# Kernel tuning notes

Hardware: AMD Instinct MI355X
Metric: run time of the kernel (lower is better)

Reference implementation:

```python
import jax, jax.numpy as jnp
import numpy as np

N_NODES = 100000
N_EDGES = 6400000
N_GRAPHS = 64


def setup_inputs() -> dict:
    key = jax.random.key(0)
    k = jax.random.split(key, 7)
    x = jax.random.normal(k[0], (N_NODES, 1), dtype=jnp.float32)
    edge_index = jax.random.randint(k[1], (2, N_EDGES), 0, N_NODES, dtype=jnp.int64)
    batch = jnp.sort(jax.random.randint(k[2], (N_NODES,), 0, N_GRAPHS, dtype=jnp.int64))
    W1 = jax.random.normal(k[3], (1, 16), dtype=jnp.float32)
    b1 = jax.random.normal(k[4], (16,), dtype=jnp.float32)
    W2 = jax.random.normal(k[5], (16, 2), dtype=jnp.float32)
    b2 = jax.random.normal(k[6], (2,), dtype=jnp.float32)
    return {"x": x, "edge_index": edge_index, "batch": batch,
            "W1": W1, "b1": b1, "W2": W2, "b2": b2}


def _gcn_layer(x, W, b, src, dst, n_nodes, dinv):
    # h = X W  (tiny feature dims)
    h = x @ W
    # symmetric normalization: norm_e = deg^-1/2[src] * deg^-1/2[dst]
    norm = dinv[src] * dinv[dst]
    msg = h[src] * norm[:, None]                 # [E+N, d] edge gather
    out = jnp.zeros((n_nodes, h.shape[1]), h.dtype).at[dst].add(msg)  # scatter-add at targets
    return out + b


def reference(x, edge_index, batch, W1, b1, W2, b2):
    n = x.shape[0]
    loops = jnp.arange(n, dtype=edge_index.dtype)
    # PyG GCNConv: add self-loops once; flow source_to_target (aggregate at edge_index[1])
    src = jnp.concatenate([edge_index[0], loops])
    dst = jnp.concatenate([edge_index[1], loops])
    deg = jnp.zeros(n, x.dtype).at[dst].add(jnp.ones((), x.dtype))
    dinv = jnp.where(deg > 0, jax.lax.rsqrt(deg), 0.0)

    h = _gcn_layer(x, W1, b1, src, dst, n, dinv)   # [N,16]
    h = _gcn_layer(h, W2, b2, src, dst, n, dinv)   # [N,2]

    # global_mean_pool over graphs
    g = N_GRAPHS
    sums = jnp.zeros((g, h.shape[1]), h.dtype).at[batch].add(h)
    counts = jnp.zeros(g, h.dtype).at[batch].add(jnp.ones((), h.dtype))
    return sums / jnp.maximum(counts, 1.0)[:, None]   # [G,2]
```

## Files before the change

kernel.cpp:

```cpp
#include <hip/hip_runtime.h>

#define N_NODES  100000
#define N_EDGES  6400000
#define N_GRAPHS 64
#define SCAN_BS  1024
#define NRDF     100096
#define DEGW     (NRDF / 4)
#define NR2      50048
#define LDSW     (NR2 / 2)
#define NR3      33344

__device__ __forceinline__ int idx_stride(const int* ei) {
    int allzero = 1;
    #pragma unroll
    for (int k = 0; k < 16; ++k)
        if (ei[2 * k + 1] != 0) allzero = 0;
    return allzero ? 2 : 1;
}

__global__ __launch_bounds__(SCAN_BS)
void deg_scan(const int* ei, unsigned char* copies) {
    __shared__ unsigned bins[DEGW];
    for (int i = threadIdx.x; i < DEGW; i += SCAN_BS) bins[i] = 0u;
    __syncthreads();
    const int stride = idx_stride(ei);
    const int tid = blockIdx.x * SCAN_BS + threadIdx.x;
    const int nth = gridDim.x * SCAN_BS;
#define DEGADD(u) { unsigned a = (unsigned)(u); \
    if (a < NRDF) atomicAdd(&bins[a >> 2], 1u << (8 * (a & 3))); }
    if (stride == 2) {
        const int4* dp = (const int4*)(ei + (size_t)N_EDGES * 2);
        const int lim = N_EDGES / 2;
        int q = tid;
        for (; q + 7 * nth < lim; q += 8 * nth) {
            int4 v0 = dp[q],           v1 = dp[q + nth];
            int4 v2 = dp[q + 2 * nth], v3 = dp[q + 3 * nth];
            int4 v4 = dp[q + 4 * nth], v5 = dp[q + 5 * nth];
            int4 v6 = dp[q + 6 * nth], v7 = dp[q + 7 * nth];
            DEGADD(v0.x); DEGADD(v0.z); DEGADD(v1.x); DEGADD(v1.z);
            DEGADD(v2.x); DEGADD(v2.z); DEGADD(v3.x); DEGADD(v3.z);
            DEGADD(v4.x); DEGADD(v4.z); DEGADD(v5.x); DEGADD(v5.z);
            DEGADD(v6.x); DEGADD(v6.z); DEGADD(v7.x); DEGADD(v7.z);
        }
        for (; q < lim; q += nth) { int4 v = dp[q]; DEGADD(v.x); DEGADD(v.z); }
    } else {
        const int4* dp = (const int4*)(ei + (size_t)N_EDGES);
        for (int q = tid; q < N_EDGES / 4; q += nth) {
            int4 v = dp[q];
            DEGADD(v.x); DEGADD(v.y); DEGADD(v.z); DEGADD(v.w);
        }
    }
#undef DEGADD
    __syncthreads();
    unsigned* my = (unsigned*)(copies + (size_t)blockIdx.x * NRDF);
    for (int i = threadIdx.x; i < DEGW; i += SCAN_BS) my[i] = bins[i];
}

__global__ void deg_merge(const unsigned char* copies, int C, const int* ei,
                          const float* x, const int* batch,
                          float* wx, float2* pbt) {
    __shared__ float red[256];
    int il = threadIdx.x & 63, cs = threadIdx.x >> 6;
    int gi = blockIdx.x * 64 + il;
    bool ok = (gi < N_NODES);
    float partial = 0.0f;
    if (ok)
        for (int c = cs; c < C; c += 4)
            partial += (float)copies[(size_t)c * NRDF + gi];
    red[threadIdx.x] = partial;
    __syncthreads();
    if (cs == 0 && ok) {
        float d = 1.0f + red[il] + red[64 + il] + red[128 + il] + red[192 + il];
        float di = rsqrtf(d);
        wx[gi] = di * x[gi];
        const int stride = idx_stride(ei);
        pbt[gi] = make_float2(di, (float)batch[(size_t)gi * stride]);
    }
}

__device__ __forceinline__ void pk_add_f16(unsigned ldsBase, unsigned a, float v) {
    _Float16 h = (_Float16)v;
    unsigned hb = (unsigned)__builtin_bit_cast(unsigned short, h);
    unsigned pk = (a & 1) ? (hb << 16) : hb;
    unsigned addr = ldsBase + ((a >> 1) << 2);
    asm volatile("ds_pk_add_f16 %0, %1" :: "v"(addr), "v"(pk) : "memory");
}

__global__ __launch_bounds__(SCAN_BS)
void acc1_scan(const int* ei, const float* wx, int G, unsigned* copies) {
    __shared__ unsigned bins[LDSW];
    for (int i = threadIdx.x; i < LDSW; i += SCAN_BS) bins[i] = 0u;
    __syncthreads();
    const int grp = (blockIdx.x >= G) ? 1 : 0;
    const int lo = grp * NR2;
    const int lb = blockIdx.x - grp * G;
    const unsigned ldsBase = (unsigned)(uintptr_t)&bins[0];
    const int stride = idx_stride(ei);
    const int tid = lb * SCAN_BS + threadIdx.x;
    const int nth = G * SCAN_BS;
    if (stride == 2) {
        const int4* sp = (const int4*)ei;
        const int4* dp = (const int4*)(ei + (size_t)N_EDGES * 2);
        const int lim = N_EDGES / 2;
        int q = tid;
        for (; q + 3 * nth < lim; q += 4 * nth) {
            int4 d0 = dp[q],           d1 = dp[q + nth];
            int4 d2 = dp[q + 2 * nth], d3 = dp[q + 3 * nth];
            int4 s0 = sp[q],           s1 = sp[q + nth];
            int4 s2 = sp[q + 2 * nth], s3 = sp[q + 3 * nth];
            unsigned a0 = (unsigned)(d0.x - lo), a1 = (unsigned)(d0.z - lo);
            unsigned a2 = (unsigned)(d1.x - lo), a3 = (unsigned)(d1.z - lo);
            unsigned a4 = (unsigned)(d2.x - lo), a5 = (unsigned)(d2.z - lo);
            unsigned a6 = (unsigned)(d3.x - lo), a7 = (unsigned)(d3.z - lo);
            float w0 = (a0 < NR2) ? wx[s0.x] : 0.0f;
            float w1 = (a1 < NR2) ? wx[s0.z] : 0.0f;
            float w2 = (a2 < NR2) ? wx[s1.x] : 0.0f;
            float w3 = (a3 < NR2) ? wx[s1.z] : 0.0f;
            float w4 = (a4 < NR2) ? wx[s2.x] : 0.0f;
            float w5 = (a5 < NR2) ? wx[s2.z] : 0.0f;
            float w6 = (a6 < NR2) ? wx[s3.x] : 0.0f;
            float w7 = (a7 < NR2) ? wx[s3.z] : 0.0f;
            if (a0 < NR2) pk_add_f16(ldsBase, a0, w0);
            if (a1 < NR2) pk_add_f16(ldsBase, a1, w1);
            if (a2 < NR2) pk_add_f16(ldsBase, a2, w2);
            if (a3 < NR2) pk_add_f16(ldsBase, a3, w3);
            if (a4 < NR2) pk_add_f16(ldsBase, a4, w4);
            if (a5 < NR2) pk_add_f16(ldsBase, a5, w5);
            if (a6 < NR2) pk_add_f16(ldsBase, a6, w6);
            if (a7 < NR2) pk_add_f16(ldsBase, a7, w7);
        }
        for (; q < lim; q += nth) {
            int4 dv = dp[q]; int4 sv = sp[q];
            unsigned a = (unsigned)(dv.x - lo), b = (unsigned)(dv.z - lo);
            if (a < NR2) pk_add_f16(ldsBase, a, wx[sv.x]);
            if (b < NR2) pk_add_f16(ldsBase, b, wx[sv.z]);
        }
    } else {
        const int4* sp = (const int4*)ei;
        const int4* dp = (const int4*)(ei + (size_t)N_EDGES);
        for (int q = tid; q < N_EDGES / 4; q += nth) {
            int4 dv = dp[q]; int4 sv = sp[q];
            unsigned a = (unsigned)(dv.x - lo), b = (unsigned)(dv.y - lo);
            unsigned c = (unsigned)(dv.z - lo), d = (unsigned)(dv.w - lo);
            if (a < NR2) pk_add_f16(ldsBase, a, wx[sv.x]);
            if (b < NR2) pk_add_f16(ldsBase, b, wx[sv.y]);
            if (c < NR2) pk_add_f16(ldsBase, c, wx[sv.z]);
            if (d < NR2) pk_add_f16(ldsBase, d, wx[sv.w]);
        }
    }
    __syncthreads();
    unsigned* my = copies + (size_t)blockIdx.x * LDSW;
    for (int i = threadIdx.x; i < LDSW; i += SCAN_BS) my[i] = bins[i];
}

__global__ void acc1_merge(const unsigned* copies, int G,
                           const float* wx, const float2* pbt,
                           float* y1, unsigned* pyz, float* gacc) {
    __shared__ float red[256];
    int t = threadIdx.x;
    if (blockIdx.x == 0 && t < 3 * N_GRAPHS) gacc[t] = 0.0f;
    int il = t & 63, cs = t >> 6;
    int gi = blockIdx.x * 64 + il;
    bool ok = (gi < N_NODES);
    float partial = 0.0f;
    int grp = (gi >= NR2) ? 1 : 0;
    int li  = gi - grp * NR2;
    if (ok) {
        int sh = 16 * (li & 1), w = li >> 1;
        const unsigned* base = copies + (size_t)grp * G * LDSW;
        for (int c = cs; c < G; c += 4) {
            unsigned u = (base[(size_t)c * LDSW + w] >> sh) & 0xFFFFu;
            partial += (float)__builtin_bit_cast(_Float16, (unsigned short)u);
        }
    }
    red[t] = partial;
    __syncthreads();
    if (cs == 0 && ok) {
        float a1 = red[il] + red[64 + il] + red[128 + il] + red[192 + il];
        float di = pbt[gi].x;
        float y1v = di * (a1 + wx[gi]);
        y1[gi] = y1v;
        _Float16 hy = (_Float16)(di * y1v);
        _Float16 hz = (_Float16)di;
        pyz[gi] = (unsigned)__builtin_bit_cast(unsigned short, hy)
                | ((unsigned)__builtin_bit_cast(unsigned short, hz) << 16);
    }
}

__global__ __launch_bounds__(SCAN_BS)
void acc2_scan(const int* ei, const unsigned* pyz, int G, unsigned* copies) {
    __shared__ unsigned bins[NR3];
    for (int i = threadIdx.x; i < NR3; i += SCAN_BS) bins[i] = 0u;
    __syncthreads();
    const int grp = blockIdx.x / G;
    const int lo = grp * NR3;
    const int lb = blockIdx.x - grp * G;
    const unsigned ldsBase = (unsigned)(uintptr_t)&bins[0];
    const int stride = idx_stride(ei);
    const int tid = lb * SCAN_BS + threadIdx.x;
    const int nth = G * SCAN_BS;
#define PKW(addr_a, pk) asm volatile("ds_pk_add_f16 %0, %1" :: \
    "v"(ldsBase + ((addr_a) << 2)), "v"(pk) : "memory")
    if (stride == 2) {
        const int4* sp = (const int4*)ei;
        const int4* dp = (const int4*)(ei + (size_t)N_EDGES * 2);
        const int lim = N_EDGES / 2;
        int q = tid;
        for (; q + 3 * nth < lim; q += 4 * nth) {
            int4 d0 = dp[q],           d1 = dp[q + nth];
            int4 d2 = dp[q + 2 * nth], d3 = dp[q + 3 * nth];
            int4 s0 = sp[q],           s1 = sp[q + nth];
            int4 s2 = sp[q + 2 * nth], s3 = sp[q + 3 * nth];
            unsigned a0 = (unsigned)(d0.x - lo), a1 = (unsigned)(d0.z - lo);
            unsigned a2 = (unsigned)(d1.x - lo), a3 = (unsigned)(d1.z - lo);
            unsigned a4 = (unsigned)(d2.x - lo), a5 = (unsigned)(d2.z - lo);
            unsigned a6 = (unsigned)(d3.x - lo), a7 = (unsigned)(d3.z - lo);
            unsigned p0 = (a0 < NR3) ? pyz[s0.x] : 0u;
            unsigned p1 = (a1 < NR3) ? pyz[s0.z] : 0u;
            unsigned p2 = (a2 < NR3) ? pyz[s1.x] : 0u;
            unsigned p3 = (a3 < NR3) ? pyz[s1.z] : 0u;
            unsigned p4 = (a4 < NR3) ? pyz[s2.x] : 0u;
            unsigned p5 = (a5 < NR3) ? pyz[s2.z] : 0u;
            unsigned p6 = (a6 < NR3) ? pyz[s3.x] : 0u;
            unsigned p7 = (a7 < NR3) ? pyz[s3.z] : 0u;
            if (a0 < NR3) PKW(a0, p0);
            if (a1 < NR3) PKW(a1, p1);
            if (a2 < NR3) PKW(a2, p2);
            if (a3 < NR3) PKW(a3, p3);
            if (a4 < NR3) PKW(a4, p4);
            if (a5 < NR3) PKW(a5, p5);
            if (a6 < NR3) PKW(a6, p6);
            if (a7 < NR3) PKW(a7, p7);
        }
        for (; q < lim; q += nth) {
            int4 dv = dp[q]; int4 sv = sp[q];
            unsigned a = (unsigned)(dv.x - lo), b = (unsigned)(dv.z - lo);
            if (a < NR3) { unsigned p = pyz[sv.x]; PKW(a, p); }
            if (b < NR3) { unsigned p = pyz[sv.z]; PKW(b, p); }
        }
    } else {
        const int4* sp = (const int4*)ei;
        const int4* dp = (const int4*)(ei + (size_t)N_EDGES);
        for (int q = tid; q < N_EDGES / 4; q += nth) {
            int4 dv = dp[q]; int4 sv = sp[q];
            unsigned a = (unsigned)(dv.x - lo), b = (unsigned)(dv.y - lo);
            unsigned c = (unsigned)(dv.z - lo), d = (unsigned)(dv.w - lo);
            if (a < NR3) { unsigned p = pyz[sv.x]; PKW(a, p); }
            if (b < NR3) { unsigned p = pyz[sv.y]; PKW(b, p); }
            if (c < NR3) { unsigned p = pyz[sv.z]; PKW(c, p); }
            if (d < NR3) { unsigned p = pyz[sv.w]; PKW(d, p); }
        }
    }
#undef PKW
    __syncthreads();
    unsigned* my = copies + (size_t)blockIdx.x * NR3;
    for (int i = threadIdx.x; i < NR3; i += SCAN_BS) my[i] = bins[i];
}

__global__ void acc2_merge(const unsigned* copies, int G,
                           const float* y1, const float2* pbt, float* gacc) {
    __shared__ float redY[256];
    __shared__ float redZ[256];
    __shared__ float bins[3 * N_GRAPHS];
    int t = threadIdx.x;
    for (int k = t; k < 3 * N_GRAPHS; k += 256) bins[k] = 0.0f;
    int il = t & 63, cs = t >> 6;
    int gi = blockIdx.x * 64 + il;
    bool ok = (gi < N_NODES);
    float pyv = 0.0f, pzv = 0.0f;
    if (ok) {
        int grp = gi / NR3;
        int li  = gi - grp * NR3;
        const unsigned* base = copies + (size_t)grp * G * NR3;
        for (int c = cs; c < G; c += 4) {
            unsigned u = base[(size_t)c * NR3 + li];
            pyv += (float)__builtin_bit_cast(_Float16, (unsigned short)(u & 0xFFFFu));
            pzv += (float)__builtin_bit_cast(_Float16, (unsigned short)(u >> 16));
        }
    }
    redY[t] = pyv;
    redZ[t] = pzv;
    __syncthreads();
    if (cs == 0 && ok) {
        float a2 = redY[il] + redY[64 + il] + redY[128 + il] + redY[192 + il];
        float az = redZ[il] + redZ[64 + il] + redZ[128 + il] + redZ[192 + il];
        float2 pb = pbt[gi];
        float di = pb.x;
        int g = (int)pb.y;
        float di2 = di * di;
        float yv = di * a2 + di2 * y1[gi];
        float zv = di * az + di2;
        atomicAdd(&bins[g], yv);
        atomicAdd(&bins[N_GRAPHS + g], zv);
        atomicAdd(&bins[2 * N_GRAPHS + g], 1.0f);
    }
    __syncthreads();
    for (int k = t; k < 3 * N_GRAPHS; k += 256)
        if (bins[k] != 0.0f) atomicAdd(&gacc[k], bins[k]);
}

__global__ void final_kernel(const float* W1, const float* b1, const float* W2,
                             const float* b2, const float* gacc, float* out) {
    int g = threadIdx.x;
    if (g >= N_GRAPHS) return;
    float w0 = 0.f, w1 = 0.f, c0 = 0.f, c1 = 0.f;
    for (int j = 0; j < 16; ++j) {
        float a = W2[2 * j], b = W2[2 * j + 1];
        w0 += W1[j] * a;  w1 += W1[j] * b;
        c0 += b1[j] * a;  c1 += b1[j] * b;
    }
    float sy  = gacc[g];
    float sz  = gacc[N_GRAPHS + g];
    float cnt = gacc[2 * N_GRAPHS + g];
    float inv = 1.0f / fmaxf(cnt, 1.0f);
    out[2 * g + 0] = (sy * w0 + sz * c0 + cnt * b2[0]) * inv;
    out[2 * g + 1] = (sy * w1 + sz * c1 + cnt * b2[1]) * inv;
}

extern "C" void kernel_launch(void* const* d_in, const int* in_sizes, int n_in,
                              void* d_out, int out_size, void* d_ws, size_t ws_size,
                              hipStream_t stream) {
    const float* x     = (const float*)d_in[0];
    const int*   ei    = (const int*)d_in[1];
    const int*   batch = (const int*)d_in[2];
    const float* W1    = (const float*)d_in[3];
    const float* b1    = (const float*)d_in[4];
    const float* W2    = (const float*)d_in[5];
    const float* b2    = (const float*)d_in[6];
    float* out = (float*)d_out;

    float*    f    = (float*)d_ws;
    float*    wx   = f;
    float*    y1   = wx + N_NODES;
    float2*   pbt  = (float2*)(y1 + N_NODES);
    unsigned* pyz  = (unsigned*)(pbt + N_NODES);
    float*    gacc = (float*)(pyz + N_NODES);
    unsigned* copies = (unsigned*)(gacc + 3 * N_GRAPHS + 16);

    const long fixedB = (5L * N_NODES + 3 * N_GRAPHS + 16) * 4;
    long availB = (long)ws_size - fixedB;
    long CD = availB / NRDF;
    if (CD > 256) CD = 256; if (CD < 8) CD = 8;
    long G1 = availB / (2L * LDSW * 4);
    if (G1 > 128) G1 = 128; if (G1 < 4) G1 = 4;
    long G2 = availB / (3L * NR3 * 4);
    if (G2 > 85) G2 = 85; if (G2 < 4) G2 = 4;

    deg_scan<<<(int)CD, SCAN_BS, 0, stream>>>(ei, (unsigned char*)copies);
    deg_merge<<<(N_NODES + 63) / 64, 256, 0, stream>>>(
        (const unsigned char*)copies, (int)CD, ei, x, batch, wx, pbt);

    acc1_scan<<<(int)(2 * G1), SCAN_BS, 0, stream>>>(ei, wx, (int)G1, copies);
    acc1_merge<<<(N_NODES + 63) / 64, 256, 0, stream>>>(
        copies, (int)G1, wx, pbt, y1, pyz, gacc);

    acc2_scan<<<(int)(3 * G2), SCAN_BS, 0, stream>>>(ei, pyz, (int)G2, copies);
    acc2_merge<<<(N_NODES + 63) / 64, 256, 0, stream>>>(
        copies, (int)G2, y1, pbt, gacc);

    final_kernel<<<1, 64, 0, stream>>>(W1, b1, W2, b2, gacc, out);
}
```

Baseline: 158.3 us.

## Compact int64 edge indices to packed int32 columns during degree pass

Measured after the change: 173.0 us. 9.3% more time.

```diff
diff --git a/kernel.cpp b/kernel.cpp
--- a/kernel.cpp
+++ b/kernel.cpp
@@ -16,6 +16,159 @@
     for (int k = 0; k < 16; ++k)
         if (ei[2 * k + 1] != 0) allzero = 0;
     return allzero ? 2 : 1;
+}
+
+__device__ __forceinline__ void pk_add_f16(unsigned ldsBase, unsigned a, float v) {
+    _Float16 h = (_Float16)v;
+    unsigned hb = (unsigned)__builtin_bit_cast(unsigned short, h);
+    unsigned pk = (a & 1) ? (hb << 16) : hb;
+    unsigned addr = ldsBase + ((a >> 1) << 2);
+    asm volatile("ds_pk_add_f16 %0, %1" :: "v"(addr), "v"(pk) : "memory");
+}
+
+__global__ __launch_bounds__(SCAN_BS)
+void pack_deg(const int* ei, unsigned* dstc, unsigned* srcc,
+              unsigned char* copies) {
+    __shared__ unsigned bins[DEGW];
+    for (int i = threadIdx.x; i < DEGW; i += SCAN_BS) bins[i] = 0u;
+    __syncthreads();
+    const int stride = idx_stride(ei);
+    const int tid = blockIdx.x * SCAN_BS + threadIdx.x;
+    const int nth = gridDim.x * SCAN_BS;
+#define DEGADD(u) { unsigned a = (unsigned)(u); \
+    if (a < NRDF) atomicAdd(&bins[a >> 2], 1u << (8 * (a & 3))); }
+    if (stride == 2) {
+        const int4* dp = (const int4*)(ei + (size_t)N_EDGES * 2);
+        const int4* sp = (const int4*)ei;
+        uint2* d2 = (uint2*)dstc;
+        uint2* s2 = (uint2*)srcc;
+        for (int q = tid; q < N_EDGES / 2; q += nth) {
+            int4 dv = dp[q], sv = sp[q];
+            DEGADD(dv.x); DEGADD(dv.z);
+            d2[q] = make_uint2((unsigned)dv.x, (unsigned)dv.z);
+            s2[q] = make_uint2((unsigned)sv.x, (unsigned)sv.z);
+        }
+    } else {
+        const int4* dp = (const int4*)(ei + (size_t)N_EDGES);
+        const int4* sp = (const int4*)ei;
+        int4* d4 = (int4*)dstc;
+        int4* s4 = (int4*)srcc;
+        for (int q = tid; q < N_EDGES / 4; q += nth) {
+            int4 dv = dp[q], sv = sp[q];
+            DEGADD(dv.x); DEGADD(dv.y); DEGADD(dv.z); DEGADD(dv.w);
+            d4[q] = dv;
+            s4[q] = sv;
+        }
+    }
+#undef DEGADD
+    __syncthreads();
+    unsigned* my = (unsigned*)(copies + (size_t)blockIdx.x * NRDF);
+    for (int i = threadIdx.x; i < DEGW; i += SCAN_BS) my[i] = bins[i];
+}
+
+__global__ __launch_bounds__(SCAN_BS)
+void acc1_scanP(const unsigned* dstc, const unsigned* srcc, const float* wx,
+                int G, unsigned* copies) {
+    __shared__ unsigned bins[LDSW];
+    for (int i = threadIdx.x; i < LDSW; i += SCAN_BS) bins[i] = 0u;
+    __syncthreads();
+    const int grp = (blockIdx.x >= G) ? 1 : 0;
+    const int lo = grp * NR2;
+    const int lb = blockIdx.x - grp * G;
+    const unsigned ldsBase = (unsigned)(uintptr_t)&bins[0];
+    const int tid = lb * SCAN_BS + threadIdx.x;
+    const int nth = G * SCAN_BS;
+    const uint4* dp = (const uint4*)dstc;
+    const uint4* sp = (const uint4*)srcc;
+    const int lim = N_EDGES / 4;
+    int q = tid;
+    for (; q + nth < lim; q += 2 * nth) {
+        uint4 d0 = dp[q], d1 = dp[q + nth];
+        uint4 s0 = sp[q], s1 = sp[q + nth];
+        unsigned a0 = d0.x - lo, a1 = d0.y - lo, a2 = d0.z - lo, a3 = d0.w - lo;
+        unsigned a4 = d1.x - lo, a5 = d1.y - lo, a6 = d1.z - lo, a7 = d1.w - lo;
+        float w0 = (a0 < NR2) ? wx[s0.x] : 0.0f;
+        float w1 = (a1 < NR2) ? wx[s0.y] : 0.0f;
+        float w2 = (a2 < NR2) ? wx[s0.z] : 0.0f;
+        float w3 = (a3 < NR2) ? wx[s0.w] : 0.0f;
+        float w4 = (a4 < NR2) ? wx[s1.x] : 0.0f;
+        float w5 = (a5 < NR2) ? wx[s1.y] : 0.0f;
+        float w6 = (a6 < NR2) ? wx[s1.z] : 0.0f;
+        float w7 = (a7 < NR2) ? wx[s1.w] : 0.0f;
+        if (a0 < NR2) pk_add_f16(ldsBase, a0, w0);
+        if (a1 < NR2) pk_add_f16(ldsBase, a1, w1);
+        if (a2 < NR2) pk_add_f16(ldsBase, a2, w2);
+        if (a3 < NR2) pk_add_f16(ldsBase, a3, w3);
+        if (a4 < NR2) pk_add_f16(ldsBase, a4, w4);
+        if (a5 < NR2) pk_add_f16(ldsBase, a5, w5);
+        if (a6 < NR2) pk_add_f16(ldsBase, a6, w6);
+        if (a7 < NR2) pk_add_f16(ldsBase, a7, w7);
+    }
+    for (; q < lim; q += nth) {
+        uint4 dv = dp[q]; uint4 sv = sp[q];
+        unsigned a = dv.x - lo, b = dv.y - lo, c = dv.z - lo, d = dv.w - lo;
+        if (a < NR2) pk_add_f16(ldsBase, a, wx[sv.x]);
+        if (b < NR2) pk_add_f16(ldsBase, b, wx[sv.y]);
+        if (c < NR2) pk_add_f16(ldsBase, c, wx[sv.z]);
+        if (d < NR2) pk_add_f16(ldsBase, d, wx[sv.w]);
+    }
+    __syncthreads();
+    unsigned* my = copies + (size_t)blockIdx.x * LDSW;
+    for (int i = threadIdx.x; i < LDSW; i += SCAN_BS) my[i] = bins[i];
+}
+
+__global__ __launch_bounds__(SCAN_BS)
+void acc2_scanP(const unsigned* dstc, const unsigned* srcc, const unsigned* pyz,
+                int G, unsigned* copies) {
+    __shared__ unsigned bins[NR3];
+    for (int i = threadIdx.x; i < NR3; i += SCAN_BS) bins[i] = 0u;
+    __syncthreads();
+    const int grp = blockIdx.x / G;
+    const int lo = grp * NR3;
+    const int lb = blockIdx.x - grp * G;
+    const unsigned ldsBase = (unsigned)(uintptr_t)&bins[0];
+    const int tid = lb * SCAN_BS + threadIdx.x;
+    const int nth = G * SCAN_BS;
+#define PKW(addr_a, pk) asm volatile("ds_pk_add_f16 %0, %1" :: \
+    "v"(ldsBase + ((addr_a) << 2)), "v"(pk) : "memory")
+    const uint4* dp = (const uint4*)dstc;
+    const uint4* sp = (const uint4*)srcc;
+    const int lim = N_EDGES / 4;
+    int q = tid;
+    for (; q + nth < lim; q += 2 * nth) {
+        uint4 d0 = dp[q], d1 = dp[q + nth];
+        uint4 s0 = sp[q], s1 = sp[q + nth];
+        unsigned a0 = d0.x - lo, a1 = d0.y - lo, a2 = d0.z - lo, a3 = d0.w - lo;
+        unsigned a4 = d1.x - lo, a5 = d1.y - lo, a6 = d1.z - lo, a7 = d1.w - lo;
+        unsigned p0 = (a0 < NR3) ? pyz[s0.x] : 0u;
+        unsigned p1 = (a1 < NR3) ? pyz[s0.y] : 0u;
+        unsigned p2 = (a2 < NR3) ? pyz[s0.z] : 0u;
+        unsigned p3 = (a3 < NR3) ? pyz[s0.w] : 0u;
+        unsigned p4 = (a4 < NR3) ? pyz[s1.x] : 0u;
+        unsigned p5 = (a5 < NR3) ? pyz[s1.y] : 0u;
+        unsigned p6 = (a6 < NR3) ? pyz[s1.z] : 0u;
+        unsigned p7 = (a7 < NR3) ? pyz[s1.w] : 0u;
+        if (a0 < NR3) PKW(a0, p0);
+        if (a1 < NR3) PKW(a1, p1);
+        if (a2 < NR3) PKW(a2, p2);
+        if (a3 < NR3) PKW(a3, p3);
+        if (a4 < NR3) PKW(a4, p4);
+        if (a5 < NR3) PKW(a5, p5);
+        if (a6 < NR3) PKW(a6, p6);
+        if (a7 < NR3) PKW(a7, p7);
+    }
+    for (; q < lim; q += nth) {
+        uint4 dv = dp[q]; uint4 sv = sp[q];
+        unsigned a = dv.x - lo, b = dv.y - lo, c = dv.z - lo, d = dv.w - lo;
+        if (a < NR3) { unsigned p = pyz[sv.x]; PKW(a, p); }
+        if (b < NR3) { unsigned p = pyz[sv.y]; PKW(b, p); }
+        if (c < NR3) { unsigned p = pyz[sv.z]; PKW(c, p); }
+        if (d < NR3) { unsigned p = pyz[sv.w]; PKW(d, p); }
+    }
+#undef PKW
+    __syncthreads();
+    unsigned* my = copies + (size_t)blockIdx.x * NR3;
+    for (int i = threadIdx.x; i < NR3; i += SCAN_BS) my[i] = bins[i];
 }
 
 __global__ __launch_bounds__(SCAN_BS)
@@ -54,36 +207,6 @@
     __syncthreads();
     unsigned* my = (unsigned*)(copies + (size_t)blockIdx.x * NRDF);
     for (int i = threadIdx.x; i < DEGW; i += SCAN_BS) my[i] = bins[i];
-}
-
-__global__ void deg_merge(const unsigned char* copies, int C, const int* ei,
-                          const float* x, const int* batch,
-                          float* wx, float2* pbt) {
-    __shared__ float red[256];
-    int il = threadIdx.x & 63, cs = threadIdx.x >> 6;
-    int gi = blockIdx.x * 64 + il;
-    bool ok = (gi < N_NODES);
-    float partial = 0.0f;
-    if (ok)
-        for (int c = cs; c < C; c += 4)
-            partial += (float)copies[(size_t)c * NRDF + gi];
-    red[threadIdx.x] = partial;
-    __syncthreads();
-    if (cs == 0 && ok) {
-        float d = 1.0f + red[il] + red[64 + il] + red[128 + il] + red[192 + il];
-        float di = rsqrtf(d);
-        wx[gi] = di * x[gi];
-        const int stride = idx_stride(ei);
-        pbt[gi] = make_float2(di, (float)batch[(size_t)gi * stride]);
-    }
-}
-
-__device__ __forceinline__ void pk_add_f16(unsigned ldsBase, unsigned a, float v) {
-    _Float16 h = (_Float16)v;
-    unsigned hb = (unsigned)__builtin_bit_cast(unsigned short, h);
-    unsigned pk = (a & 1) ? (hb << 16) : hb;
-    unsigned addr = ldsBase + ((a >> 1) << 2);
-    asm volatile("ds_pk_add_f16 %0, %1" :: "v"(addr), "v"(pk) : "memory");
 }
 
 __global__ __launch_bounds__(SCAN_BS)
@@ -151,40 +274,6 @@
     __syncthreads();
     unsigned* my = copies + (size_t)blockIdx.x * LDSW;
     for (int i = threadIdx.x; i < LDSW; i += SCAN_BS) my[i] = bins[i];
-}
-
-__global__ void acc1_merge(const unsigned* copies, int G,
-                           const float* wx, const float2* pbt,
-                           float* y1, unsigned* pyz, float* gacc) {
-    __shared__ float red[256];
-    int t = threadIdx.x;
-    if (blockIdx.x == 0 && t < 3 * N_GRAPHS) gacc[t] = 0.0f;
-    int il = t & 63, cs = t >> 6;
-    int gi = blockIdx.x * 64 + il;
-    bool ok = (gi < N_NODES);
-    float partial = 0.0f;
-    int grp = (gi >= NR2) ? 1 : 0;
-    int li  = gi - grp * NR2;
-    if (ok) {
-        int sh = 16 * (li & 1), w = li >> 1;
-        const unsigned* base = copies + (size_t)grp * G * LDSW;
-        for (int c = cs; c < G; c += 4) {
-            unsigned u = (base[(size_t)c * LDSW + w] >> sh) & 0xFFFFu;
-            partial += (float)__builtin_bit_cast(_Float16, (unsigned short)u);
-        }
-    }
-    red[t] = partial;
-    __syncthreads();
-    if (cs == 0 && ok) {
-        float a1 = red[il] + red[64 + il] + red[128 + il] + red[192 + il];
-        float di = pbt[gi].x;
-        float y1v = di * (a1 + wx[gi]);
-        y1[gi] = y1v;
-        _Float16 hy = (_Float16)(di * y1v);
-        _Float16 hz = (_Float16)di;
-        pyz[gi] = (unsigned)__builtin_bit_cast(unsigned short, hy)
-                | ((unsigned)__builtin_bit_cast(unsigned short, hz) << 16);
-    }
 }
 
 __global__ __launch_bounds__(SCAN_BS)
@@ -257,6 +346,62 @@
     for (int i = threadIdx.x; i < NR3; i += SCAN_BS) my[i] = bins[i];
 }
 
+__global__ void deg_merge(const unsigned char* copies, int C, const int* ei,
+                          const float* x, const int* batch,
+                          float* wx, float2* pbt) {
+    __shared__ float red[256];
+    int il = threadIdx.x & 63, cs = threadIdx.x >> 6;
+    int gi = blockIdx.x * 64 + il;
+    bool ok = (gi < N_NODES);
+    float partial = 0.0f;
+    if (ok)
+        for (int c = cs; c < C; c += 4)
+            partial += (float)copies[(size_t)c * NRDF + gi];
+    red[threadIdx.x] = partial;
+    __syncthreads();
+    if (cs == 0 && ok) {
+        float d = 1.0f + red[il] + red[64 + il] + red[128 + il] + red[192 + il];
+        float di = rsqrtf(d);
+        wx[gi] = di * x[gi];
+        const int stride = idx_stride(ei);
+        pbt[gi] = make_float2(di, (float)batch[(size_t)gi * stride]);
+    }
+}
+
+__global__ void acc1_merge(const unsigned* copies, int G,
+                           const float* wx, const float2* pbt,
+                           float* y1, unsigned* pyz, float* gacc) {
+    __shared__ float red[256];
+    int t = threadIdx.x;
+    if (blockIdx.x == 0 && t < 3 * N_GRAPHS) gacc[t] = 0.0f;
+    int il = t & 63, cs = t >> 6;
+    int gi = blockIdx.x * 64 + il;
+    bool ok = (gi < N_NODES);
+    float partial = 0.0f;
+    int grp = (gi >= NR2) ? 1 : 0;
+    int li  = gi - grp * NR2;
+    if (ok) {
+        int sh = 16 * (li & 1), w = li >> 1;
+        const unsigned* base = copies + (size_t)grp * G * LDSW;
+        for (int c = cs; c < G; c += 4) {
+            unsigned u = (base[(size_t)c * LDSW + w] >> sh) & 0xFFFFu;
+            partial += (float)__builtin_bit_cast(_Float16, (unsigned short)u);
+        }
+    }
+    red[t] = partial;
+    __syncthreads();
+    if (cs == 0 && ok) {
+        float a1 = red[il] + red[64 + il] + red[128 + il] + red[192 + il];
+        float di = pbt[gi].x;
+        float y1v = di * (a1 + wx[gi]);
+        y1[gi] = y1v;
+        _Float16 hy = (_Float16)(di * y1v);
+        _Float16 hz = (_Float16)di;
+        pyz[gi] = (unsigned)__builtin_bit_cast(unsigned short, hy)
+                | ((unsigned)__builtin_bit_cast(unsigned short, hz) << 16);
+    }
+}
+
 __global__ void acc2_merge(const unsigned* copies, int G,
                            const float* y1, const float2* pbt, float* gacc) {
     __shared__ float redY[256];
@@ -335,28 +480,53 @@
     float2*   pbt  = (float2*)(y1 + N_NODES);
     unsigned* pyz  = (unsigned*)(pbt + N_NODES);
     float*    gacc = (float*)(pyz + N_NODES);
-    unsigned* copies = (unsigned*)(gacc + 3 * N_GRAPHS + 16);
+    unsigned* after = (unsigned*)(gacc + 3 * N_GRAPHS + 16);
 
     const long fixedB = (5L * N_NODES + 3 * N_GRAPHS + 16) * 4;
-    long availB = (long)ws_size - fixedB;
-    long CD = availB / NRDF;
-    if (CD > 256) CD = 256; if (CD < 8) CD = 8;
-    long G1 = availB / (2L * LDSW * 4);
-    if (G1 > 128) G1 = 128; if (G1 < 4) G1 = 4;
-    long G2 = availB / (3L * NR3 * 4);
-    if (G2 > 85) G2 = 85; if (G2 < 4) G2 = 4;
-
-    deg_scan<<<(int)CD, SCAN_BS, 0, stream>>>(ei, (unsigned char*)copies);
-    deg_merge<<<(N_NODES + 63) / 64, 256, 0, stream>>>(
-        (const unsigned char*)copies, (int)CD, ei, x, batch, wx, pbt);
-
-    acc1_scan<<<(int)(2 * G1), SCAN_BS, 0, stream>>>(ei, wx, (int)G1, copies);
-    acc1_merge<<<(N_NODES + 63) / 64, 256, 0, stream>>>(
-        copies, (int)G1, wx, pbt, y1, pyz, gacc);
-
-    acc2_scan<<<(int)(3 * G2), SCAN_BS, 0, stream>>>(ei, pyz, (int)G2, copies);
-    acc2_merge<<<(N_NODES + 63) / 64, 256, 0, stream>>>(
-        copies, (int)G2, y1, pbt, gacc);
-
+    const long packedColsB = 2L * N_EDGES * 4;
+    const long copiesMaxB  = 3L * 85 * NR3 * 4;
+    const bool packed = (long)ws_size >= fixedB + packedColsB + copiesMaxB
+                                         + (1L << 20);
+
+    if (packed) {
+        unsigned* dstc = after;
+        unsigned* srcc = dstc + N_EDGES;
+        unsigned* copies = srcc + N_EDGES;
+        const int CD = 256, G1 = 128, G2 = 85;
+
+        pack_deg<<<CD, SCAN_BS, 0, stream>>>(ei, dstc, srcc,
+                                             (unsigned char*)copies);
+        deg_merge<<<(N_NODES + 63) / 64, 256, 0, stream>>>(
+            (const unsigned char*)copies, CD, ei, x, batch, wx, pbt);
+
+        acc1_scanP<<<2 * G1, SCAN_BS, 0, stream>>>(dstc, srcc, wx, G1, copies);
+        acc1_merge<<<(N_NODES + 63) / 64, 256, 0, stream>>>(
+            copies, G1, wx, pbt, y1, pyz, gacc);
+
+        acc2_scanP<<<3 * G2, SCAN_BS, 0, stream>>>(dstc, srcc, pyz, G2, copies);
+        acc2_merge<<<(N_NODES + 63) / 64, 256, 0, stream>>>(
+            copies, G2, y1, pbt, gacc);
+    } else {
+        unsigned* copies = after;
+        long availB = (long)ws_size - fixedB;
+        long CD = availB / NRDF;
+        if (CD > 256) CD = 256; if (CD < 8) CD = 8;
+        long G1 = availB / (2L * LDSW * 4);
+        if (G1 > 128) G1 = 128; if (G1 < 4) G1 = 4;
+        long G2 = availB / (3L * NR3 * 4);
+        if (G2 > 85) G2 = 85; if (G2 < 4) G2 = 4;
+
+        deg_scan<<<(int)CD, SCAN_BS, 0, stream>>>(ei, (unsigned char*)copies);
+        deg_merge<<<(N_NODES + 63) / 64, 256, 0, stream>>>(
+            (const unsigned char*)copies, (int)CD, ei, x, batch, wx, pbt);
+
+        acc1_scan<<<(int)(2 * G1), SCAN_BS, 0, stream>>>(ei, wx, (int)G1, copies);
+        acc1_merge<<<(N_NODES + 63) / 64, 256, 0, stream>>>(
+            copies, (int)G1, wx, pbt, y1, pyz, gacc);
+
+        acc2_scan<<<(int)(3 * G2), SCAN_BS, 0, stream>>>(ei, pyz, (int)G2, copies);
+        acc2_merge<<<(N_NODES + 63) / 64, 256, 0, stream>>>(
+            copies, (int)G2, y1, pbt, gacc);
+    }
     final_kernel<<<1, 64, 0, stream>>>(W1, b1, W2, b2, gacc, out);
 }
```
